# Optimization experiments

Hardware: AMD Instinct MI355X
Metric: run time of the kernel (lower is better)

The kernel has to match this reference:

```python
import jax, jax.numpy as jnp
import numpy as np

N_HEADS = 8
N_LAYERS = 2
LN_EPS = 1e-5


def _mha(x, Win, bin_, Wout, bout):
    # torch nn.MultiheadAttention, eval mode (dropout off). x: [b, s, d]
    b, s, d = x.shape
    dh = d // N_HEADS
    qkv = x @ Win.T + bin_                      # [b, s, 3d]
    q, k, v = jnp.split(qkv, 3, axis=-1)
    q = q.reshape(b, s, N_HEADS, dh)
    k = k.reshape(b, s, N_HEADS, dh)
    v = v.reshape(b, s, N_HEADS, dh)
    scores = jnp.einsum('bqhd,bkhd->bhqk', q, k) / jnp.sqrt(jnp.asarray(dh, x.dtype))
    attn = jax.nn.softmax(scores, axis=-1)
    o = jnp.einsum('bhqk,bkhd->bqhd', attn, v).reshape(b, s, d)
    return o @ Wout.T + bout


def _layer_norm(x, g, b):
    mu = jnp.mean(x, axis=-1, keepdims=True)
    var = jnp.mean(jnp.square(x - mu), axis=-1, keepdims=True)
    return (x - mu) * jax.lax.rsqrt(var + LN_EPS) * g + b


def _vertex_conv(feat, inc, prev, Win, bin_, Wout, bout, Wproj, ln_g, ln_b, alpha):
    # feat: [b,m,d], inc: [b,m,e]
    attn = _mha(feat, Win, bin_, Wout, bout)              # [b,m,d]
    scores = jnp.einsum('bme,bmd->bed', inc, attn)        # incidence aggregation
    w = jax.nn.softmax(scores, axis=1)                    # softmax over edges
    # fused form of einsum('bme,bmd->bmed') then einsum('bmed,bed->bed')
    edge = scores * w                                     # [b,e,d]
    edge = edge @ Wproj.T                                 # no-bias projection
    edge = _layer_norm(edge, ln_g, ln_b)
    if prev is not None:
        edge = alpha * prev + (1.0 - alpha) * edge
        edge = edge + prev
    return edge


def _edge_conv(inc, edge_feat, prev, Win, bin_, Wout, bout, Wproj, ln_g, ln_b, alpha):
    # inc: [b,m,e], edge_feat: [b,e,d]
    _ = _mha(edge_feat, Win, bin_, Wout, bout)            # attn computed, output unused downstream
    wef = jnp.einsum('bed,bme->bmd', edge_feat, inc)      # edge->node aggregation
    node = wef @ Wproj.T
    node = _layer_norm(node, ln_g, ln_b)
    if prev is not None:
        node = alpha * prev + (1.0 - alpha) * node
        node = node + prev
    return node


def setup_inputs() -> dict:
    key = jax.random.key(0)
    ks = jax.random.split(key, 8)
    b, m, e, d = 8, 1024, 1536, 256
    s = 0.02
    return {
        'features': jax.random.normal(ks[0], (b, m, d), jnp.float32),
        'inc_mat': (jax.random.uniform(ks[1], (b, m, e), jnp.float32) < 0.05).astype(jnp.float32),
        'vc_Win': jax.random.normal(ks[2], (3 * d, d), jnp.float32) * s,
        'vc_bin': jnp.zeros((3 * d,), jnp.float32),
        'vc_Wout': jax.random.normal(ks[3], (d, d), jnp.float32) * s,
        'vc_bout': jnp.zeros((d,), jnp.float32),
        'vc_Wproj': jax.random.normal(ks[4], (d, d), jnp.float32) * s,
        'vc_ln_g': jnp.ones((d,), jnp.float32),
        'vc_ln_b': jnp.zeros((d,), jnp.float32),
        'vc_alpha': jnp.asarray(0.5, jnp.float32),
        'ec_Win': jax.random.normal(ks[5], (3 * d, d), jnp.float32) * s,
        'ec_bin': jnp.zeros((3 * d,), jnp.float32),
        'ec_Wout': jax.random.normal(ks[6], (d, d), jnp.float32) * s,
        'ec_bout': jnp.zeros((d,), jnp.float32),
        'ec_Wproj': jax.random.normal(ks[7], (d, d), jnp.float32) * s,
        'ec_ln_g': jnp.ones((d,), jnp.float32),
        'ec_ln_b': jnp.zeros((d,), jnp.float32),
        'ec_alpha': jnp.asarray(0.5, jnp.float32),
    }


def reference(features, inc_mat,
              vc_Win, vc_bin, vc_Wout, vc_bout, vc_Wproj, vc_ln_g, vc_ln_b, vc_alpha,
              ec_Win, ec_bin, ec_Wout, ec_bout, ec_Wproj, ec_ln_g, ec_ln_b, ec_alpha):
    vc = (vc_Win, vc_bin, vc_Wout, vc_bout, vc_Wproj, vc_ln_g, vc_ln_b, vc_alpha)
    ec = (ec_Win, ec_bin, ec_Wout, ec_bout, ec_Wproj, ec_ln_g, ec_ln_b, ec_alpha)
    edge_feats = _vertex_conv(features, inc_mat, None, *vc)
    node_feats = _edge_conv(inc_mat, edge_feats, features, *ec)
    for _ in range(N_LAYERS):  # shared weights across layers, as in the torch module
        edge_feats = _vertex_conv(features, inc_mat, edge_feats, *vc)
        node_feats = _edge_conv(inc_mat, edge_feats, node_feats, *ec)
    return node_feats, edge_feats, inc_mat
```

## Files before the change

kernel.cpp:

```cpp
#include <hip/hip_runtime.h>
#include <stdint.h>


#define DEV static __device__ __forceinline__

typedef __attribute__((ext_vector_type(8))) short bf16x8;
typedef __attribute__((ext_vector_type(4))) float f32x4;

DEV uint16_t f2bf(float x){
  union{float f; uint32_t u;} v; v.f=x;
  uint32_t r = v.u + 0x7fffu + ((v.u>>16)&1u);
  return (uint16_t)(r>>16);
}
DEV float bf2f(uint16_t b){
  union{uint32_t u; float f;} v; v.u=((uint32_t)b)<<16; return v.f;
}

#if __has_builtin(__builtin_amdgcn_global_load_lds)
#define HAVE_GLL 1
#else
#define HAVE_GLL 0
#endif

DEV void load_lds16(const uint16_t* g, void* l){
#if HAVE_GLL
  __builtin_amdgcn_global_load_lds((const __attribute__((address_space(1))) uint32_t*)g,
                                   (__attribute__((address_space(3))) uint32_t*)l, 16, 0, 0);
#else
  *(bf16x8*)l = *(const bf16x8*)g;
#endif
}

__global__ __launch_bounds__(256)
void prep(const float* __restrict__ inc, float* __restrict__ out_inc,
          uint16_t* __restrict__ incb, uint16_t* __restrict__ incT,
          const float* __restrict__ feats, const float* __restrict__ win,
          const float* __restrict__ wout, const float* __restrict__ wpv,
          const float* __restrict__ wpe,
          uint16_t* __restrict__ xb, uint16_t* __restrict__ ow,
          uint16_t* __restrict__ oo, uint16_t* __restrict__ ov,
          uint16_t* __restrict__ oe){
  __shared__ float T[32][33];
  int bx = blockIdx.x;
  int tid = threadIdx.x;
  if (bx < 12288){
    int x = bx % 48;
    int t = bx / 48;
    int y = t % 32;
    int b = t / 32;
    int c0 = x*32, r0 = y*32;
    int tx = tid & 31, ty = tid >> 5;
    size_t base = (size_t)b*1024*1536;
#pragma unroll
    for (int j=0;j<4;++j){
      int r = r0 + ty + j*8;
      size_t idx = base + (size_t)r*1536 + c0 + tx;
      float v = inc[idx];
      T[ty+j*8][tx] = v;
      out_inc[idx] = v;
      incb[idx] = f2bf(v);
    }
    __syncthreads();
    size_t baseT = (size_t)b*1536*1024;
#pragma unroll
    for (int j=0;j<4;++j){
      int c = c0 + ty + j*8;
      incT[baseT + (size_t)c*1024 + r0 + tx] = f2bf(T[tx][ty+j*8]);
    }
  } else {
    int i = (bx - 12288)*256 + tid;
    const float* src; uint16_t* dst; int j;
    if (i < 524288){ src=feats; dst=xb; j=i; }
    else {
      i -= 524288;
      if (i < 49152){ src=win; dst=ow; j=i; }
      else if (i < 65536){ src=wout; dst=oo; j=i-49152; }
      else if (i < 81920){ src=wpv; dst=ov; j=i-65536; }
      else { src=wpe; dst=oe; j=i-81920; }
    }
    float4 v = ((const float4*)src)[j];
    union { uint16_t u[4]; uint64_t q; } p;
    p.u[0]=f2bf(v.x); p.u[1]=f2bf(v.y); p.u[2]=f2bf(v.z); p.u[3]=f2bf(v.w);
    ((uint64_t*)dst)[j] = p.q;
  }
}

template<int WM, int BK, int EPI>
__global__ __launch_bounds__(256, 3)
void gemm_nt(const uint16_t* __restrict__ A, const uint16_t* __restrict__ B,
             float* __restrict__ Cf, uint16_t* __restrict__ Cb,
             const float* __restrict__ bias,
             int M, int N, int K, long sA, long sB, long sC,
             float* __restrict__ extra){
  constexpr int AROWS = WM*32;
  constexpr int UPR = BK/8;
  constexpr int RPP = 256/UPR;
  __shared__ short As[AROWS*BK];
  __shared__ short Bs[128*BK];
  const int tid = threadIdx.x;
  const int lane = tid & 63;
  const int w = tid >> 6;
  const int wm = w & 1, wn = w >> 1;
  const int r = lane & 15, q = lane >> 4;
  const long zb = blockIdx.z;
  const uint16_t* Ab = A + zb*sA + (size_t)(blockIdx.x*AROWS)*K;
  const uint16_t* Bb = B + zb*sB + (size_t)(blockIdx.y*128)*K;
  f32x4 acc[WM][4];
#pragma unroll
  for (int i=0;i<WM;++i)
#pragma unroll
    for (int j=0;j<4;++j) acc[i][j] = (f32x4){0.f,0.f,0.f,0.f};

  const int srow = tid / UPR;
  const int sblk = tid % UPR;

  for (int kb = 0; kb < K; kb += BK){
#pragma unroll
    for (int i=0;i<AROWS/RPP;++i){
      int row = srow + RPP*i;
      int lblk = sblk ^ (row & (UPR-1));
      load_lds16(Ab + (size_t)row*K + kb + lblk*8, (char*)As + i*4096 + tid*16);
    }
#pragma unroll
    for (int i=0;i<128/RPP;++i){
      int row = srow + RPP*i;
      int lblk = sblk ^ (row & (UPR-1));
      load_lds16(Bb + (size_t)row*K + kb + lblk*8, (char*)Bs + i*4096 + tid*16);
    }
    __syncthreads();
#pragma unroll
    for (int kc=0;kc<BK/32;++kc){
      bf16x8 af[WM], bf[4];
#pragma unroll
      for (int mt=0;mt<WM;++mt){
        int m = wm*(WM*16) + mt*16 + r;
        af[mt] = *(const bf16x8*)&As[m*BK + ((kc*4 + q) ^ (m&(UPR-1)))*8];
      }
#pragma unroll
      for (int nt=0;nt<4;++nt){
        int n = wn*64 + nt*16 + r;
        bf[nt] = *(const bf16x8*)&Bs[n*BK + ((kc*4 + q) ^ (n&(UPR-1)))*8];
      }
#pragma unroll
      for (int mt=0;mt<WM;++mt)
#pragma unroll
        for (int nt=0;nt<4;++nt)
          acc[mt][nt] = __builtin_amdgcn_mfma_f32_16x16x32_bf16(af[mt], bf[nt], acc[mt][nt], 0,0,0);
    }
    __syncthreads();
  }

  const int gm0 = blockIdx.x*AROWS + wm*(WM*16);
  const int gn0 = blockIdx.y*128 + wn*64;

  if constexpr (EPI == 1){
#pragma unroll
    for (int mt=0;mt<WM;++mt){
      int gmb = gm0 + mt*16 + q*4;
      size_t bb_ = (size_t)(gmb>>10)*(256*1024);
      int mm = gmb & 1023;
#pragma unroll
      for (int nt=0;nt<4;++nt){
        int gn = gn0 + nt*16 + r;
        float bv = bias ? bias[gn] : 0.f;
        union{uint16_t u[4]; uint64_t q64;} pk;
#pragma unroll
        for (int reg=0;reg<4;++reg) pk.u[reg] = f2bf(acc[mt][nt][reg] + bv);
        *(uint64_t*)(Cb + bb_ + (size_t)gn*1024 + mm) = pk.q64;
      }
    }
  } else {
#pragma unroll
    for (int mt=0;mt<WM;++mt){
#pragma unroll
      for (int nt=0;nt<4;++nt){
        int gn = gn0 + nt*16 + r;
        float bv = bias ? bias[gn] : 0.f;
#pragma unroll
        for (int reg=0;reg<4;++reg){
          int gm = gm0 + mt*16 + q*4 + reg;
          float v = acc[mt][nt][reg] + bv;
          size_t off = (size_t)(zb*sC) + (size_t)gm*N + gn;
          if (Cf) Cf[off] = v;
          if (Cb) Cb[off] = f2bf(v);
        }
      }
    }
    if constexpr (EPI == 2){
      __shared__ float colsum[2][128];
#pragma unroll
      for (int nt=0;nt<4;++nt){
        float s = 0.f;
#pragma unroll
        for (int mt=0;mt<WM;++mt)
#pragma unroll
          for (int reg=0;reg<4;++reg) s += __expf(acc[mt][nt][reg]);
        s += __shfl_xor(s, 16);
        s += __shfl_xor(s, 32);
        if (q == 0) colsum[wm][wn*64 + nt*16 + r] = s;
      }
      __syncthreads();
      if (tid < 128){
        float v = colsum[0][tid] + colsum[1][tid];
        extra[((size_t)zb*gridDim.x + blockIdx.x)*256 + blockIdx.y*128 + tid] = v;
      }
    }
  }
}

__global__ __launch_bounds__(256, 4)
void gemm_ln_edge(const uint16_t* __restrict__ SB, const uint16_t* __restrict__ B,
                  const float* __restrict__ part, const float* __restrict__ g,
                  const float* __restrict__ bb, const float* __restrict__ alpha,
                  float* __restrict__ out, uint16_t* __restrict__ baset){
  __shared__ short As[32*64];
  __shared__ short Bs[256*64];
  __shared__ float lnS[4][32], lnQ[4][32];
  __shared__ float PLinv[256];
  const int tid = threadIdx.x;
  const int lane = tid & 63;
  const int w = tid >> 6;
  const int r = lane & 15, q = lane >> 4;
  const int batch = blockIdx.x / 48;

  {
    float s = 0.f;
#pragma unroll
    for (int i=0;i<24;++i) s += part[((size_t)batch*24 + i)*256 + tid];
    PLinv[tid] = 1.0f / s;
  }
  __syncthreads();

  f32x4 acc[2][4];
#pragma unroll
  for (int i=0;i<2;++i)
#pragma unroll
    for (int j=0;j<4;++j) acc[i][j] = (f32x4){0.f,0.f,0.f,0.f};

  const int srow = tid >> 3;
  const int sblk = tid & 7;

  for (int kb = 0; kb < 256; kb += 64){
    {
      bf16x8 v = *(const bf16x8*)(SB + (size_t)(blockIdx.x*32 + srow)*256 + kb + sblk*8);
      const float* Lp = &PLinv[kb + sblk*8];
      bf16x8 pv;
#pragma unroll
      for (int j=0;j<8;++j){
        float x = bf2f((uint16_t)v[j]);
        pv[j] = (short)f2bf(x * __expf(x) * Lp[j]);
      }
      *(bf16x8*)&As[srow*64 + (sblk ^ (srow&7))*8] = pv;
    }
#pragma unroll
    for (int i=0;i<8;++i){
      int row = srow + 32*i;
      int lblk = sblk ^ (row & 7);
      load_lds16(B + (size_t)row*256 + kb + lblk*8, (char*)Bs + i*4096 + tid*16);
    }
    __syncthreads();
#pragma unroll
    for (int kc=0;kc<2;++kc){
      bf16x8 af[2], bf[4];
#pragma unroll
      for (int mt=0;mt<2;++mt){
        int m = mt*16 + r;
        af[mt] = *(const bf16x8*)&As[m*64 + ((kc*4 + q) ^ (m&7))*8];
      }
#pragma unroll
      for (int nt=0;nt<4;++nt){
        int n = w*64 + nt*16 + r;
        bf[nt] = *(const bf16x8*)&Bs[n*64 + ((kc*4 + q) ^ (n&7))*8];
      }
#pragma unroll
      for (int mt=0;mt<2;++mt)
#pragma unroll
        for (int nt=0;nt<4;++nt)
          acc[mt][nt] = __builtin_amdgcn_mfma_f32_16x16x32_bf16(af[mt], bf[nt], acc[mt][nt], 0,0,0);
    }
    __syncthreads();
  }

  float rs[2][4], rq[2][4];
#pragma unroll
  for (int mt=0;mt<2;++mt)
#pragma unroll
    for (int reg=0;reg<4;++reg){
      float s=0.f, s2=0.f;
#pragma unroll
      for (int nt=0;nt<4;++nt){
        float v = acc[mt][nt][reg];
        s += v; s2 += v*v;
      }
#pragma unroll
      for (int off=1; off<16; off<<=1){ s += __shfl_xor(s,off); s2 += __shfl_xor(s2,off); }
      rs[mt][reg]=s; rq[mt][reg]=s2;
    }
  if (r == 0){
#pragma unroll
    for (int mt=0;mt<2;++mt)
#pragma unroll
      for (int reg=0;reg<4;++reg){
        int row = mt*16 + q*4 + reg;
        lnS[w][row] = rs[mt][reg];
        lnQ[w][row] = rq[mt][reg];
      }
  }
  __syncthreads();

  const float c0 = 3.0f + alpha[0];
  float mu_[2][4], rstd_[2][4];
#pragma unroll
  for (int mt=0;mt<2;++mt)
#pragma unroll
    for (int reg=0;reg<4;++reg){
      int row = mt*16 + q*4 + reg;
      float S = lnS[0][row]+lnS[1][row]+lnS[2][row]+lnS[3][row];
      float Q = lnQ[0][row]+lnQ[1][row]+lnQ[2][row]+lnQ[3][row];
      float mu = S * (1.f/256.f);
      float var = fmaxf(Q*(1.f/256.f) - mu*mu, 0.f);
      mu_[mt][reg] = mu;
      rstd_[mt][reg] = rsqrtf(var + 1e-5f);
    }

  int e0 = (blockIdx.x % 48) * 32;
#pragma unroll
  for (int mt=0;mt<2;++mt){
#pragma unroll
    for (int nt=0;nt<4;++nt){
      int gn = w*64 + nt*16 + r;
      float gv = g[gn], bv = bb[gn];
      union{uint16_t u[4]; uint64_t q64;} pk;
#pragma unroll
      for (int reg=0;reg<4;++reg){
        int row = mt*16 + q*4 + reg;
        size_t gm = (size_t)blockIdx.x*32 + row;
        float o = ((acc[mt][nt][reg]-mu_[mt][reg])*rstd_[mt][reg]*gv + bv) * c0;
        pk.u[reg] = f2bf(o);
        out[gm*256 + gn] = o;
      }
      int ee = e0 + mt*16 + q*4;
      *(uint64_t*)(baset + ((size_t)batch*256 + gn)*1536 + ee) = pk.q64;
    }
  }
}

__global__ __launch_bounds__(256, 4)
void gemm_ln_node(const uint16_t* __restrict__ A, const uint16_t* __restrict__ B,
                  const float* __restrict__ g, const float* __restrict__ bb,
                  const float* __restrict__ alpha, const float* __restrict__ feats,
                  float* __restrict__ out){
  __shared__ short As[32*64];
  __shared__ short Bs[256*64];
  __shared__ float lnS[4][32], lnQ[4][32];
  const int tid = threadIdx.x;
  const int lane = tid & 63;
  const int w = tid >> 6;
  const int r = lane & 15, q = lane >> 4;
  const uint16_t* Ab = A + (size_t)(blockIdx.x*32)*256;
  f32x4 acc[2][4];
#pragma unroll
  for (int i=0;i<2;++i)
#pragma unroll
    for (int j=0;j<4;++j) acc[i][j] = (f32x4){0.f,0.f,0.f,0.f};

  const int srow = tid >> 3;
  const int sblk = tid & 7;

  for (int kb = 0; kb < 256; kb += 64){
    {
      int lblk = sblk ^ (srow & 7);
      load_lds16(Ab + (size_t)srow*256 + kb + lblk*8, (char*)As + tid*16);
    }
#pragma unroll
    for (int i=0;i<8;++i){
      int row = srow + 32*i;
      int lblk = sblk ^ (row & 7);
      load_lds16(B + (size_t)row*256 + kb + lblk*8, (char*)Bs + i*4096 + tid*16);
    }
    __syncthreads();
#pragma unroll
    for (int kc=0;kc<2;++kc){
      bf16x8 af[2], bf[4];
#pragma unroll
      for (int mt=0;mt<2;++mt){
        int m = mt*16 + r;
        af[mt] = *(const bf16x8*)&As[m*64 + ((kc*4 + q) ^ (m&7))*8];
      }
#pragma unroll
      for (int nt=0;nt<4;++nt){
        int n = w*64 + nt*16 + r;
        bf[nt] = *(const bf16x8*)&Bs[n*64 + ((kc*4 + q) ^ (n&7))*8];
      }
#pragma unroll
      for (int mt=0;mt<2;++mt)
#pragma unroll
        for (int nt=0;nt<4;++nt)
          acc[mt][nt] = __builtin_amdgcn_mfma_f32_16x16x32_bf16(af[mt], bf[nt], acc[mt][nt], 0,0,0);
    }
    __syncthreads();
  }

  float rs[2][4], rq[2][4];
#pragma unroll
  for (int mt=0;mt<2;++mt)
#pragma unroll
    for (int reg=0;reg<4;++reg){
      float s=0.f, s2=0.f;
#pragma unroll
      for (int nt=0;nt<4;++nt){
        float v = acc[mt][nt][reg];
        s += v; s2 += v*v;
      }
#pragma unroll
      for (int off=1; off<16; off<<=1){ s += __shfl_xor(s,off); s2 += __shfl_xor(s2,off); }
      rs[mt][reg]=s; rq[mt][reg]=s2;
    }
  if (r == 0){
#pragma unroll
    for (int mt=0;mt<2;++mt)
#pragma unroll
      for (int reg=0;reg<4;++reg){
        int row = mt*16 + q*4 + reg;
        lnS[w][row] = rs[mt][reg];
        lnQ[w][row] = rq[mt][reg];
      }
  }
  __syncthreads();

  const float a = alpha[0];
  const float ap1 = 1.f + a;
  const float cn = (1.f - a)*(ap1*ap1 + ap1 + 1.f);
  const float cf = ap1*ap1*ap1;

#pragma unroll
  for (int mt=0;mt<2;++mt){
#pragma unroll
    for (int reg=0;reg<4;++reg){
      int row = mt*16 + q*4 + reg;
      float S = lnS[0][row]+lnS[1][row]+lnS[2][row]+lnS[3][row];
      float Q = lnQ[0][row]+lnQ[1][row]+lnQ[2][row]+lnQ[3][row];
      float mu = S * (1.f/256.f);
      float var = fmaxf(Q*(1.f/256.f) - mu*mu, 0.f);
      float rstd = rsqrtf(var + 1e-5f);
      size_t gm = (size_t)blockIdx.x*32 + row;
#pragma unroll
      for (int nt=0;nt<4;++nt){
        int gn = w*64 + nt*16 + r;
        float nv = (acc[mt][nt][reg]-mu)*rstd*g[gn] + bb[gn];
        out[gm*256 + gn] = cf*feats[gm*256+gn] + cn*nv;
      }
    }
  }
}

DEV void stage_K(short* Kl, const uint16_t* __restrict__ qkv, size_t rowbase,
                 int c, int h, int kr){
  const uint16_t* kp = qkv + ((rowbase + c*256 + kr)*768 + 256 + h*32);
  int sz = (kr&3) ^ ((kr>>2)&1);
#pragma unroll
  for (int lb=0; lb<4; ++lb){
    bf16x8 v = *(const bf16x8*)(kp + lb*8);
    *(bf16x8*)&Kl[kr*32 + ((lb ^ sz))*8] = v;
  }
}

DEV void stage_V(short* VT, const uint16_t* __restrict__ qkv, size_t rowbase,
                 int c, int h, int t){
  int kvp = (t>>1)*2;
  int dhh = (t&1)*16;
  const uint16_t* v0 = qkv + ((rowbase + c*256 + kvp)*768 + 512 + h*32 + dhh);
  const uint16_t* v1 = v0 + 768;
  bf16x8 a0 = *(const bf16x8*)(v0);
  bf16x8 a1 = *(const bf16x8*)(v0+8);
  bf16x8 b0 = *(const bf16x8*)(v1);
  bf16x8 b1 = *(const bf16x8*)(v1+8);
  int blkbase = kvp>>3, off = kvp&7;
#pragma unroll
  for (int i=0;i<8;++i){
    int dh = dhh + i;
    uint32_t pack = (uint32_t)(uint16_t)a0[i] | ((uint32_t)(uint16_t)b0[i]<<16);
    *(uint32_t*)&VT[dh*256 + ((blkbase ^ (dh&7))*8) + off] = pack;
  }
#pragma unroll
  for (int i=0;i<8;++i){
    int dh = dhh + 8 + i;
    uint32_t pack = (uint32_t)(uint16_t)a1[i] | ((uint32_t)(uint16_t)b1[i]<<16);
    *(uint32_t*)&VT[dh*256 + ((blkbase ^ (dh&7))*8) + off] = pack;
  }
}

__global__ __launch_bounds__(512)
void attn_fwd(const uint16_t* __restrict__ qkv, uint16_t* __restrict__ O){
  __shared__ short Kl[256*32];
  __shared__ short VT[32*256];
  __shared__ short Pl[8][16*36];
  const int tid = threadIdx.x, lane = tid&63, w = tid>>6;
  const int r = lane&15, q = lane>>4;
  const int bh = blockIdx.y, b = bh>>3, h = bh&7;
  const int q0 = blockIdx.x*128 + w*16;
  const size_t rowbase = (size_t)b*1024;

  bf16x8 aq;
  {
    const float qscale = 0.17677669529663687f;
    const uint16_t* p = qkv + ((rowbase + q0 + r)*768 + h*32 + q*8);
    bf16x8 t = *(const bf16x8*)p;
#pragma unroll
    for (int j=0;j<8;++j)
      t[j] = (short)f2bf(bf2f((uint16_t)t[j]) * qscale);
    aq = t;
  }

  f32x4 o[2];
  o[0]=(f32x4){0.f,0.f,0.f,0.f}; o[1]=(f32x4){0.f,0.f,0.f,0.f};
  float l = 0.f;

  for (int c=0;c<4;++c){
    __syncthreads();
    if (tid < 256) stage_K(Kl, qkv, rowbase, c, h, tid);
    else           stage_V(VT, qkv, rowbase, c, h, tid-256);
    __syncthreads();
    for (int s32=0; s32<8; ++s32){
#pragma unroll
      for (int t2=0;t2<2;++t2){
        int rn = s32*32 + t2*16 + r;
        int sz = (rn&3) ^ ((rn>>2)&1);
        bf16x8 bk = *(const bf16x8*)&Kl[rn*32 + ((q ^ sz))*8];
        f32x4 z = (f32x4){0.f,0.f,0.f,0.f};
        f32x4 st = __builtin_amdgcn_mfma_f32_16x16x32_bf16(bk, aq, z, 0,0,0);
        union{uint16_t u[4]; uint64_t q64;} pk;
#pragma unroll
        for (int reg=0;reg<4;++reg){
          float p = __expf(st[reg]);
          l += p;
          pk.u[reg] = f2bf(p);
        }
        *(uint64_t*)&Pl[w][r*36 + t2*16 + q*4] = pk.q64;
      }
      bf16x8 bv[2];
#pragma unroll
      for (int db=0;db<2;++db){
        int dh = db*16 + r;
        bv[db] = *(const bf16x8*)&VT[dh*256 + (((s32*4 + q) ^ (dh&7)))*8];
      }
      bf16x8 ap = *(const bf16x8*)&Pl[w][r*36 + q*8];
#pragma unroll
      for (int db=0;db<2;++db)
        o[db] = __builtin_amdgcn_mfma_f32_16x16x32_bf16(ap, bv[db], o[db], 0,0,0);
    }
  }

  l += __shfl_xor(l, 16);
  l += __shfl_xor(l, 32);
#pragma unroll
  for (int db=0;db<2;++db)
#pragma unroll
    for (int reg=0;reg<4;++reg){
      float li = __shfl(l, q*4 + reg);
      int qr = q0 + q*4 + reg;
      O[(rowbase + qr)*256 + h*32 + db*16 + r] = f2bf(o[db][reg] / li);
    }
}

extern "C" void kernel_launch(void* const* d_in, const int* in_sizes, int n_in,
                              void* d_out, int out_size, void* d_ws, size_t ws_size,
                              hipStream_t stream){
  const float* features = (const float*)d_in[0];
  const float* inc      = (const float*)d_in[1];
  const float* vc_Win   = (const float*)d_in[2];
  const float* vc_bin   = (const float*)d_in[3];
  const float* vc_Wout  = (const float*)d_in[4];
  const float* vc_bout  = (const float*)d_in[5];
  const float* vc_Wproj = (const float*)d_in[6];
  const float* vc_ln_g  = (const float*)d_in[7];
  const float* vc_ln_b  = (const float*)d_in[8];
  const float* vc_alpha = (const float*)d_in[9];
  const float* ec_Wproj = (const float*)d_in[14];
  const float* ec_ln_g  = (const float*)d_in[15];
  const float* ec_ln_b  = (const float*)d_in[16];
  const float* ec_alpha = (const float*)d_in[17];

  float* out = (float*)d_out;
  float* out_node = out;
  float* out_edge = out + 2097152;
  float* out_inc  = out + 5242880;

  char* ws = (char*)d_ws;
  uint16_t* XB     = (uint16_t*)(ws + 0);
  float*    PART   = (float*)   (ws + 0);
  uint16_t* WINB   = (uint16_t*)(ws + 4194304);
  uint16_t* WOUTB  = (uint16_t*)(ws + 4587520);
  uint16_t* WPVB   = (uint16_t*)(ws + 4718592);
  uint16_t* WPEB   = (uint16_t*)(ws + 4849664);
  uint16_t* INCB   = (uint16_t*)(ws + 4988928);
  uint16_t* INCT   = (uint16_t*)(ws + 30154752);
  uint16_t* QKVB   = (uint16_t*)(ws + 55320576);
  uint16_t* SCORESB= (uint16_t*)(ws + 55320576);
  uint16_t* OB     = (uint16_t*)(ws + 67903488);
  uint16_t* ATTNT  = (uint16_t*)(ws + 72097792);
  uint16_t* BASET  = (uint16_t*)(ws + 82583552);
  uint16_t* W0B    = (uint16_t*)(ws + 88875008);

  prep<<<14720,256,0,stream>>>(inc, out_inc, INCB, INCT,
                               features, vc_Win, vc_Wout, vc_Wproj, ec_Wproj,
                               XB, WINB, WOUTB, WPVB, WPEB);

  gemm_nt<4,64,0><<<dim3(64,6,1),256,0,stream>>>(XB, WINB, nullptr, QKVB, vc_bin,
                                                 8192,768,256, 0,0,0, nullptr);
  attn_fwd<<<dim3(8,64),512,0,stream>>>(QKVB, OB);
  gemm_nt<2,128,1><<<dim3(128,2,1),256,0,stream>>>(OB, WOUTB, nullptr, ATTNT, vc_bout,
                                                   8192,256,256, 0,0,0, nullptr);

  gemm_nt<2,128,2><<<dim3(24,2,8),256,0,stream>>>(INCT, ATTNT, nullptr, SCORESB, nullptr,
                                                  1536,256,1024,
                                                  1536L*1024, 256L*1024, 1536L*256, PART);

  gemm_ln_edge<<<384,256,0,stream>>>(SCORESB, WPVB, PART, vc_ln_g, vc_ln_b,
                                     vc_alpha, out_edge, BASET);

  gemm_nt<2,128,0><<<dim3(16,2,8),256,0,stream>>>(INCB, BASET, nullptr, W0B, nullptr,
                                                  1024,256,1536,
                                                  1024L*1536, 256L*1536, 1024L*256, nullptr);
  gemm_ln_node<<<256,256,0,stream>>>(W0B, WPEB, ec_ln_g, ec_ln_b, ec_alpha,
                                     features, out_node);
}
```

Before: 259.3 us.

## Fuse node GEMM chain, add score GEMM kernel, exp2 softmax and block swizzles

The two node-side GEMMs (incidence×edge aggregation, then projection with layernorm) are merged into one kernel that keeps the intermediate in LDS, which removes the W0B round trip. A dedicated score GEMM writes v*exp(v) and column partial sums directly, so the edge GEMM no longer recomputes exp. Attention switches to exp2 with a log2e-folded scale and packed bf16 conversion. Block indices are remapped (swizzled) across batches in several kernels. In exchange the fused node kernel uses more LDS with launch bounds lowered to 3 blocks, and each block runs a long K=1536 loop over only 256 blocks.

```diff
diff --git a/kernel.cpp b/kernel.cpp
--- a/kernel.cpp
+++ b/kernel.cpp
@@ -15,6 +15,18 @@
 DEV float bf2f(uint16_t b){
   union{uint32_t u; float f;} v; v.u=((uint32_t)b)<<16; return v.f;
 }
+
+DEV uint32_t cvtpk_bf16(float lo, float hi){
+  uint32_t d;
+  asm("v_cvt_pk_bf16_f32 %0, %1, %2" : "=v"(d) : "v"(lo), "v"(hi));
+  return d;
+}
+
+#if __has_builtin(__builtin_amdgcn_exp2f)
+DEV float exp2fast(float x){ return __builtin_amdgcn_exp2f(x); }
+#else
+DEV float exp2fast(float x){ return __expf(x * 0.6931471805599453f); }
+#endif
 
 #if __has_builtin(__builtin_amdgcn_global_load_lds)
 #define HAVE_GLL 1
@@ -186,25 +198,85 @@
         }
       }
     }
-    if constexpr (EPI == 2){
-      __shared__ float colsum[2][128];
+  }
+  (void)extra;
+}
+
+__global__ __launch_bounds__(256, 4)
+void gemm_score(const uint16_t* __restrict__ A,
+                const uint16_t* __restrict__ B,
+                float* __restrict__ part,
+                uint16_t* __restrict__ VE){
+  __shared__ short As[32*64];
+  __shared__ short Bs[256*64];
+  const int tid = threadIdx.x;
+  const int lane = tid & 63;
+  const int w = tid >> 6;
+  const int r = lane & 15, q = lane >> 4;
+  const int bx = (blockIdx.x & 7)*48 + (blockIdx.x >> 3);
+  const int batch = bx / 48;
+  const uint16_t* Ab = A + (size_t)bx*32*1024;
+  const uint16_t* Bb = B + (size_t)batch*256*1024;
+
+  f32x4 acc[2][4];
+#pragma unroll
+  for (int i=0;i<2;++i)
+#pragma unroll
+    for (int j=0;j<4;++j) acc[i][j] = (f32x4){0.f,0.f,0.f,0.f};
+
+  const int srow = tid >> 3;
+  const int sblk = tid & 7;
+
+  for (int kb = 0; kb < 1024; kb += 64){
+    { int lblk = sblk ^ (srow & 7);
+      load_lds16(Ab + (size_t)srow*1024 + kb + lblk*8, (char*)As + tid*16); }
+#pragma unroll
+    for (int i=0;i<8;++i){
+      int row = srow + 32*i;
+      int lblk = sblk ^ (row & 7);
+      load_lds16(Bb + (size_t)row*1024 + kb + lblk*8, (char*)Bs + i*4096 + tid*16);
+    }
+    __syncthreads();
+#pragma unroll
+    for (int kc=0;kc<2;++kc){
+      bf16x8 af[2], bf[4];
+#pragma unroll
+      for (int mt=0;mt<2;++mt){
+        int m = mt*16 + r;
+        af[mt] = *(const bf16x8*)&As[m*64 + ((kc*4 + q) ^ (m&7))*8];
+      }
 #pragma unroll
       for (int nt=0;nt<4;++nt){
-        float s = 0.f;
-#pragma unroll
-        for (int mt=0;mt<WM;++mt)
-#pragma unroll
-          for (int reg=0;reg<4;++reg) s += __expf(acc[mt][nt][reg]);
-        s += __shfl_xor(s, 16);
-        s += __shfl_xor(s, 32);
-        if (q == 0) colsum[wm][wn*64 + nt*16 + r] = s;
-      }
-      __syncthreads();
-      if (tid < 128){
-        float v = colsum[0][tid] + colsum[1][tid];
-        extra[((size_t)zb*gridDim.x + blockIdx.x)*256 + blockIdx.y*128 + tid] = v;
-      }
-    }
+        int n = w*64 + nt*16 + r;
+        bf[nt] = *(const bf16x8*)&Bs[n*64 + ((kc*4 + q) ^ (n&7))*8];
+      }
+#pragma unroll
+      for (int mt=0;mt<2;++mt)
+#pragma unroll
+        for (int nt=0;nt<4;++nt)
+          acc[mt][nt] = __builtin_amdgcn_mfma_f32_16x16x32_bf16(af[mt], bf[nt], acc[mt][nt], 0,0,0);
+    }
+    __syncthreads();
+  }
+
+#pragma unroll
+  for (int nt=0;nt<4;++nt){
+    int gn = w*64 + nt*16 + r;
+    float s = 0.f;
+#pragma unroll
+    for (int mt=0;mt<2;++mt){
+#pragma unroll
+      for (int reg=0;reg<4;++reg){
+        float v = acc[mt][nt][reg];
+        float ev = __expf(v);
+        s += ev;
+        int row = mt*16 + q*4 + reg;
+        VE[(size_t)(bx*32 + row)*256 + gn] = f2bf(v*ev);
+      }
+    }
+    s += __shfl_xor(s, 16);
+    s += __shfl_xor(s, 32);
+    if (q == 0) part[(size_t)bx*256 + gn] = s;
   }
 }
 
@@ -221,12 +293,13 @@
   const int lane = tid & 63;
   const int w = tid >> 6;
   const int r = lane & 15, q = lane >> 4;
-  const int batch = blockIdx.x / 48;
+  const int bx = (blockIdx.x & 7)*48 + (blockIdx.x >> 3);
+  const int batch = bx / 48;
 
   {
     float s = 0.f;
 #pragma unroll
-    for (int i=0;i<24;++i) s += part[((size_t)batch*24 + i)*256 + tid];
+    for (int i=0;i<48;++i) s += part[((size_t)batch*48 + i)*256 + tid];
     PLinv[tid] = 1.0f / s;
   }
   __syncthreads();
@@ -242,15 +315,17 @@
 
   for (int kb = 0; kb < 256; kb += 64){
     {
-      bf16x8 v = *(const bf16x8*)(SB + (size_t)(blockIdx.x*32 + srow)*256 + kb + sblk*8);
+      bf16x8 v = *(const bf16x8*)(SB + (size_t)(bx*32 + srow)*256 + kb + sblk*8);
       const float* Lp = &PLinv[kb + sblk*8];
-      bf16x8 pv;
-#pragma unroll
-      for (int j=0;j<8;++j){
-        float x = bf2f((uint16_t)v[j]);
-        pv[j] = (short)f2bf(x * __expf(x) * Lp[j]);
-      }
-      *(bf16x8*)&As[srow*64 + (sblk ^ (srow&7))*8] = pv;
+      float xv[8];
+#pragma unroll
+      for (int j=0;j<8;++j) xv[j] = bf2f((uint16_t)v[j]) * Lp[j];
+      union{uint32_t u[4]; bf16x8 v8;} pk;
+      pk.u[0] = cvtpk_bf16(xv[0], xv[1]);
+      pk.u[1] = cvtpk_bf16(xv[2], xv[3]);
+      pk.u[2] = cvtpk_bf16(xv[4], xv[5]);
+      pk.u[3] = cvtpk_bf16(xv[6], xv[7]);
+      *(bf16x8*)&As[srow*64 + (sblk ^ (srow&7))*8] = pk.v8;
     }
 #pragma unroll
     for (int i=0;i<8;++i){
@@ -323,7 +398,7 @@
       rstd_[mt][reg] = rsqrtf(var + 1e-5f);
     }
 
-  int e0 = (blockIdx.x % 48) * 32;
+  int e0 = (bx % 48) * 32;
 #pragma unroll
   for (int mt=0;mt<2;++mt){
 #pragma unroll
@@ -334,7 +409,7 @@
 #pragma unroll
       for (int reg=0;reg<4;++reg){
         int row = mt*16 + q*4 + reg;
-        size_t gm = (size_t)blockIdx.x*32 + row;
+        size_t gm = (size_t)bx*32 + row;
         float o = ((acc[mt][nt][reg]-mu_[mt][reg])*rstd_[mt][reg]*gv + bv) * c0;
         pk.u[reg] = f2bf(o);
         out[gm*256 + gn] = o;
@@ -345,86 +420,141 @@
   }
 }
 
-__global__ __launch_bounds__(256, 4)
-void gemm_ln_node(const uint16_t* __restrict__ A, const uint16_t* __restrict__ B,
-                  const float* __restrict__ g, const float* __restrict__ bb,
-                  const float* __restrict__ alpha, const float* __restrict__ feats,
-                  float* __restrict__ out){
-  __shared__ short As[32*64];
-  __shared__ short Bs[256*64];
-  __shared__ float lnS[4][32], lnQ[4][32];
+__global__ __launch_bounds__(256, 3)
+void gemm_node_fused(const uint16_t* __restrict__ inc,
+                     const uint16_t* __restrict__ baset,
+                     const uint16_t* __restrict__ wpe,
+                     const float* __restrict__ g, const float* __restrict__ bb,
+                     const float* __restrict__ alpha,
+                     const float* __restrict__ feats, float* __restrict__ out){
+  __shared__ short Ws[256*64];
+  __shared__ short As2[32*256];
+  __shared__ short Is[32*64];
   const int tid = threadIdx.x;
   const int lane = tid & 63;
   const int w = tid >> 6;
   const int r = lane & 15, q = lane >> 4;
-  const uint16_t* Ab = A + (size_t)(blockIdx.x*32)*256;
-  f32x4 acc[2][4];
-#pragma unroll
-  for (int i=0;i<2;++i)
-#pragma unroll
-    for (int j=0;j<4;++j) acc[i][j] = (f32x4){0.f,0.f,0.f,0.f};
+  const int bx = (blockIdx.x & 7)*32 + (blockIdx.x >> 3);
+  const int batch = bx >> 5;
+  const int mt0 = (bx & 31) * 32;
 
   const int srow = tid >> 3;
   const int sblk = tid & 7;
 
-  for (int kb = 0; kb < 256; kb += 64){
-    {
-      int lblk = sblk ^ (srow & 7);
-      load_lds16(Ab + (size_t)srow*256 + kb + lblk*8, (char*)As + tid*16);
-    }
+  const uint16_t* Bb = baset + (size_t)batch*256*1536;
+  const uint16_t* Ib = inc + ((size_t)batch*1024 + mt0)*1536;
+
+  f32x4 acc1[4][2];
+#pragma unroll
+  for (int i=0;i<4;++i)
+#pragma unroll
+    for (int j=0;j<2;++j) acc1[i][j] = (f32x4){0.f,0.f,0.f,0.f};
+
+  for (int kb = 0; kb < 1536; kb += 64){
 #pragma unroll
     for (int i=0;i<8;++i){
       int row = srow + 32*i;
       int lblk = sblk ^ (row & 7);
-      load_lds16(B + (size_t)row*256 + kb + lblk*8, (char*)Bs + i*4096 + tid*16);
-    }
+      load_lds16(Bb + (size_t)row*1536 + kb + lblk*8, (char*)Ws + i*4096 + tid*16);
+    }
+    { int lblk = sblk ^ (srow & 7);
+      load_lds16(Ib + (size_t)srow*1536 + kb + lblk*8, (char*)Is + tid*16); }
     __syncthreads();
 #pragma unroll
     for (int kc=0;kc<2;++kc){
-      bf16x8 af[2], bf[4];
-#pragma unroll
-      for (int mt=0;mt<2;++mt){
-        int m = mt*16 + r;
-        af[mt] = *(const bf16x8*)&As[m*64 + ((kc*4 + q) ^ (m&7))*8];
-      }
-#pragma unroll
-      for (int nt=0;nt<4;++nt){
-        int n = w*64 + nt*16 + r;
-        bf[nt] = *(const bf16x8*)&Bs[n*64 + ((kc*4 + q) ^ (n&7))*8];
-      }
-#pragma unroll
-      for (int mt=0;mt<2;++mt)
-#pragma unroll
-        for (int nt=0;nt<4;++nt)
-          acc[mt][nt] = __builtin_amdgcn_mfma_f32_16x16x32_bf16(af[mt], bf[nt], acc[mt][nt], 0,0,0);
-    }
-    __syncthreads();
-  }
-
-  float rs[2][4], rq[2][4];
-#pragma unroll
-  for (int mt=0;mt<2;++mt)
-#pragma unroll
-    for (int reg=0;reg<4;++reg){
-      float s=0.f, s2=0.f;
-#pragma unroll
-      for (int nt=0;nt<4;++nt){
-        float v = acc[mt][nt][reg];
+      bf16x8 af[4], bf[2];
+#pragma unroll
+      for (int mt=0;mt<4;++mt){
+        int d = w*64 + mt*16 + r;
+        af[mt] = *(const bf16x8*)&Ws[d*64 + ((kc*4 + q) ^ (d&7))*8];
+      }
+#pragma unroll
+      for (int nt=0;nt<2;++nt){
+        int m = nt*16 + r;
+        bf[nt] = *(const bf16x8*)&Is[m*64 + ((kc*4 + q) ^ (m&7))*8];
+      }
+#pragma unroll
+      for (int mt=0;mt<4;++mt)
+#pragma unroll
+        for (int nt=0;nt<2;++nt)
+          acc1[mt][nt] = __builtin_amdgcn_mfma_f32_16x16x32_bf16(af[mt], bf[nt], acc1[mt][nt], 0,0,0);
+    }
+    __syncthreads();
+  }
+
+#pragma unroll
+  for (int mt=0;mt<4;++mt){
+    int j = w*8 + mt*2 + (q>>1);
+#pragma unroll
+    for (int nt=0;nt<2;++nt){
+      int m = nt*16 + r;
+      union{uint16_t u[4]; uint64_t q64;} pk;
+#pragma unroll
+      for (int reg=0;reg<4;++reg) pk.u[reg] = f2bf(acc1[mt][nt][reg]);
+      *(uint64_t*)((char*)As2 + m*512 + ((j ^ (m&7))<<4) + ((q&1)<<3)) = pk.q64;
+    }
+  }
+
+  f32x4 acc2[4][2];
+#pragma unroll
+  for (int i=0;i<4;++i)
+#pragma unroll
+    for (int j=0;j<2;++j) acc2[i][j] = (f32x4){0.f,0.f,0.f,0.f};
+
+  for (int kb = 0; kb < 256; kb += 64){
+#pragma unroll
+    for (int i=0;i<8;++i){
+      int row = srow + 32*i;
+      int lblk = sblk ^ (row & 7);
+      load_lds16(wpe + (size_t)row*256 + kb + lblk*8, (char*)Ws + i*4096 + tid*16);
+    }
+    __syncthreads();
+#pragma unroll
+    for (int kc=0;kc<2;++kc){
+      bf16x8 af[4], bf[2];
+#pragma unroll
+      for (int mt=0;mt<4;++mt){
+        int dp = w*64 + mt*16 + r;
+        af[mt] = *(const bf16x8*)&Ws[dp*64 + ((kc*4 + q) ^ (dp&7))*8];
+      }
+#pragma unroll
+      for (int nt=0;nt<2;++nt){
+        int m = nt*16 + r;
+        int jr = (kb>>3) + kc*4 + q;
+        bf[nt] = *(const bf16x8*)((char*)As2 + m*512 + ((jr ^ (m&7))<<4));
+      }
+#pragma unroll
+      for (int mt=0;mt<4;++mt)
+#pragma unroll
+        for (int nt=0;nt<2;++nt)
+          acc2[mt][nt] = __builtin_amdgcn_mfma_f32_16x16x32_bf16(af[mt], bf[nt], acc2[mt][nt], 0,0,0);
+    }
+    __syncthreads();
+  }
+
+  float* lnS = (float*)Is;
+  float* lnQ = lnS + 128;
+  float s_[2], q_[2];
+#pragma unroll
+  for (int nt=0;nt<2;++nt){
+    float s=0.f, s2=0.f;
+#pragma unroll
+    for (int mt=0;mt<4;++mt)
+#pragma unroll
+      for (int reg=0;reg<4;++reg){
+        float v = acc2[mt][nt][reg];
         s += v; s2 += v*v;
       }
-#pragma unroll
-      for (int off=1; off<16; off<<=1){ s += __shfl_xor(s,off); s2 += __shfl_xor(s2,off); }
-      rs[mt][reg]=s; rq[mt][reg]=s2;
-    }
-  if (r == 0){
-#pragma unroll
-    for (int mt=0;mt<2;++mt)
-#pragma unroll
-      for (int reg=0;reg<4;++reg){
-        int row = mt*16 + q*4 + reg;
-        lnS[w][row] = rs[mt][reg];
-        lnQ[w][row] = rq[mt][reg];
-      }
+    s += __shfl_xor(s,16); s2 += __shfl_xor(s2,16);
+    s += __shfl_xor(s,32); s2 += __shfl_xor(s2,32);
+    s_[nt]=s; q_[nt]=s2;
+  }
+  if (q == 0){
+#pragma unroll
+    for (int nt=0;nt<2;++nt){
+      lnS[w*32 + nt*16 + r] = s_[nt];
+      lnQ[w*32 + nt*16 + r] = q_[nt];
+    }
   }
   __syncthreads();
 
@@ -433,23 +563,34 @@
   const float cn = (1.f - a)*(ap1*ap1 + ap1 + 1.f);
   const float cf = ap1*ap1*ap1;
 
-#pragma unroll
-  for (int mt=0;mt<2;++mt){
-#pragma unroll
-    for (int reg=0;reg<4;++reg){
-      int row = mt*16 + q*4 + reg;
-      float S = lnS[0][row]+lnS[1][row]+lnS[2][row]+lnS[3][row];
-      float Q = lnQ[0][row]+lnQ[1][row]+lnQ[2][row]+lnQ[3][row];
-      float mu = S * (1.f/256.f);
-      float var = fmaxf(Q*(1.f/256.f) - mu*mu, 0.f);
-      float rstd = rsqrtf(var + 1e-5f);
-      size_t gm = (size_t)blockIdx.x*32 + row;
-#pragma unroll
-      for (int nt=0;nt<4;++nt){
-        int gn = w*64 + nt*16 + r;
-        float nv = (acc[mt][nt][reg]-mu)*rstd*g[gn] + bb[gn];
-        out[gm*256 + gn] = cf*feats[gm*256+gn] + cn*nv;
-      }
+  float mu_[2], rstd_[2];
+#pragma unroll
+  for (int nt=0;nt<2;++nt){
+    int col = nt*16 + r;
+    float S = lnS[col] + lnS[32+col] + lnS[64+col] + lnS[96+col];
+    float Q = lnQ[col] + lnQ[32+col] + lnQ[64+col] + lnQ[96+col];
+    float mu = S * (1.f/256.f);
+    float var = fmaxf(Q*(1.f/256.f) - mu*mu, 0.f);
+    mu_[nt] = mu;
+    rstd_[nt] = rsqrtf(var + 1e-5f);
+  }
+
+#pragma unroll
+  for (int mt=0;mt<4;++mt){
+    int dp0 = w*64 + mt*16 + q*4;
+    float4 gv = *(const float4*)&g[dp0];
+    float4 bv = *(const float4*)&bb[dp0];
+#pragma unroll
+    for (int nt=0;nt<2;++nt){
+      int m = nt*16 + r;
+      size_t gm = (size_t)batch*1024 + mt0 + m;
+      float4 fv = *(const float4*)&feats[gm*256 + dp0];
+      float4 ov;
+      ov.x = cf*fv.x + cn*((acc2[mt][nt][0]-mu_[nt])*rstd_[nt]*gv.x + bv.x);
+      ov.y = cf*fv.y + cn*((acc2[mt][nt][1]-mu_[nt])*rstd_[nt]*gv.y + bv.y);
+      ov.z = cf*fv.z + cn*((acc2[mt][nt][2]-mu_[nt])*rstd_[nt]*gv.z + bv.z);
+      ov.w = cf*fv.w + cn*((acc2[mt][nt][3]-mu_[nt])*rstd_[nt]*gv.w + bv.w);
+      *(float4*)&out[gm*256 + dp0] = ov;
     }
   }
 }
@@ -497,13 +638,15 @@
   __shared__ short Pl[8][16*36];
   const int tid = threadIdx.x, lane = tid&63, w = tid>>6;
   const int r = lane&15, q = lane>>4;
-  const int bh = blockIdx.y, b = bh>>3, h = bh&7;
-  const int q0 = blockIdx.x*128 + w*16;
+  const int logical = (blockIdx.x & 7)*64 + (blockIdx.x >> 3);
+  const int bh = logical >> 3, qc = logical & 7;
+  const int b = bh>>3, h = bh&7;
+  const int q0 = qc*128 + w*16;
   const size_t rowbase = (size_t)b*1024;
 
   bf16x8 aq;
   {
-    const float qscale = 0.17677669529663687f;
+    const float qscale = 0.25505654380651023f;
     const uint16_t* p = qkv + ((rowbase + q0 + r)*768 + h*32 + q*8);
     bf16x8 t = *(const bf16x8*)p;
 #pragma unroll
@@ -529,13 +672,14 @@
         bf16x8 bk = *(const bf16x8*)&Kl[rn*32 + ((q ^ sz))*8];
         f32x4 z = (f32x4){0.f,0.f,0.f,0.f};
         f32x4 st = __builtin_amdgcn_mfma_f32_16x16x32_bf16(bk, aq, z, 0,0,0);
-        union{uint16_t u[4]; uint64_t q64;} pk;
-#pragma unroll
-        for (int reg=0;reg<4;++reg){
-          float p = __expf(st[reg]);
-          l += p;
-          pk.u[reg] = f2bf(p);
-        }
+        float p0 = exp2fast(st[0]);
+        float p1 = exp2fast(st[1]);
+        float p2 = exp2fast(st[2]);
+        float p3 = exp2fast(st[3]);
+        l += (p0+p1)+(p2+p3);
+        union{uint32_t u[2]; uint64_t q64;} pk;
+        pk.u[0] = cvtpk_bf16(p0, p1);
+        pk.u[1] = cvtpk_bf16(p2, p3);
         *(uint64_t*)&Pl[w][r*36 + t2*16 + q*4] = pk.q64;
       }
       bf16x8 bv[2];
@@ -600,7 +744,6 @@
   uint16_t* OB     = (uint16_t*)(ws + 67903488);
   uint16_t* ATTNT  = (uint16_t*)(ws + 72097792);
   uint16_t* BASET  = (uint16_t*)(ws + 82583552);
-  uint16_t* W0B    = (uint16_t*)(ws + 88875008);
 
   prep<<<14720,256,0,stream>>>(inc, out_inc, INCB, INCT,
                                features, vc_Win, vc_Wout, vc_Wproj, ec_Wproj,
@@ -608,20 +751,15 @@
 
   gemm_nt<4,64,0><<<dim3(64,6,1),256,0,stream>>>(XB, WINB, nullptr, QKVB, vc_bin,
                                                  8192,768,256, 0,0,0, nullptr);
-  attn_fwd<<<dim3(8,64),512,0,stream>>>(QKVB, OB);
+  attn_fwd<<<512,512,0,stream>>>(QKVB, OB);
   gemm_nt<2,128,1><<<dim3(128,2,1),256,0,stream>>>(OB, WOUTB, nullptr, ATTNT, vc_bout,
                                                    8192,256,256, 0,0,0, nullptr);
 
-  gemm_nt<2,128,2><<<dim3(24,2,8),256,0,stream>>>(INCT, ATTNT, nullptr, SCORESB, nullptr,
-                                                  1536,256,1024,
-                                                  1536L*1024, 256L*1024, 1536L*256, PART);
+  gemm_score<<<384,256,0,stream>>>(INCT, ATTNT, PART, SCORESB);
 
   gemm_ln_edge<<<384,256,0,stream>>>(SCORESB, WPVB, PART, vc_ln_g, vc_ln_b,
                                      vc_alpha, out_edge, BASET);
 
-  gemm_nt<2,128,0><<<dim3(16,2,8),256,0,stream>>>(INCB, BASET, nullptr, W0B, nullptr,
-                                                  1024,256,1536,
-                                                  1024L*1536, 256L*1536, 1024L*256, nullptr);
-  gemm_ln_node<<<256,256,0,stream>>>(W0B, WPEB, ec_ln_g, ec_ln_b, ec_alpha,
-                                     features, out_node);
-}
+  gemm_node_fused<<<256,256,0,stream>>>(INCB, BASET, WPEB, ec_ln_g, ec_ln_b,
+                                        ec_alpha, features, out_node);
+}
```

Result: no change. 256.7 us (-1.0%).
